# Kernel optimization log

Measured on AMD Instinct MI355X. Metric: run time of the kernel, lower is better.

Reference implementation:

```python
import jax, jax.numpy as jnp
import numpy as np

B, S, H, V = 4, 512, 256, 32000


def setup_inputs() -> dict:
    key = jax.random.key(0)
    ks = jax.random.split(key, 6)
    s = 0.02
    x = jax.random.randint(ks[0], (B, S), 0, V)
    emb = jax.random.normal(ks[1], (V, H), dtype=jnp.float32) * s
    W_ih = jax.random.normal(ks[2], (3 * H, H), dtype=jnp.float32) * s
    W_hh = jax.random.normal(ks[3], (3 * H, H), dtype=jnp.float32) * s
    b_ih = jnp.zeros((3 * H,), jnp.float32)
    b_hh = jnp.zeros((3 * H,), jnp.float32)
    W_out = jax.random.normal(ks[4], (V, H), dtype=jnp.float32) * s
    b_out = jnp.zeros((V,), jnp.float32)
    return dict(x=x, emb=emb, W_ih=W_ih, W_hh=W_hh, b_ih=b_ih, b_hh=b_hh,
                W_out=W_out, b_out=b_out)


def gru_sequence(embedded, W_ih, W_hh, b_ih, b_hh):
    # embedded: [B, S, H]; precompute all input projections once: [B, S, 3H]
    xp = jnp.einsum('bsh,gh->bsg', embedded, W_ih) + b_ih
    Hdim = W_hh.shape[1]
    h0 = jnp.zeros((embedded.shape[0], Hdim), embedded.dtype)

    def step(h, xt):  # xt: [B, 3H]
        hp = h @ W_hh.T + b_hh  # [B, 3H]
        xr, xz, xn = jnp.split(xt, 3, axis=-1)
        hr, hz, hn = jnp.split(hp, 3, axis=-1)
        r = jax.nn.sigmoid(xr + hr)
        z = jax.nn.sigmoid(xz + hz)
        n = jnp.tanh(xn + r * hn)
        h_new = (1.0 - z) * n + z * h
        return h_new, h_new

    _, hs = jax.lax.scan(step, h0, jnp.swapaxes(xp, 0, 1))  # [S, B, H]
    return jnp.swapaxes(hs, 0, 1)  # [B, S, H]


def reference(x, emb, W_ih, W_hh, b_ih, b_hh, W_out, b_out):
    embedded = emb[x]                                   # [B, S, H]
    rnn_out = gru_sequence(embedded, W_ih, W_hh, b_ih, b_hh)
    logits = jnp.einsum('bsh,vh->bsv', rnn_out, W_out) + b_out  # [B, S, V]
    # symbolic constraint: if prev token == 0, tokens >= 3 are invalid (t > 0)
    prev_zero = (x[:, :-1] == 0)                        # [B, S-1]
    prev_zero = jnp.pad(prev_zero, ((0, 0), (1, 0)))    # t=0 never masked
    vocab_ge3 = jnp.arange(logits.shape[-1]) >= 3       # [V]
    invalid = prev_zero[:, :, None] & vocab_ge3[None, None, :]
    return jnp.where(invalid, -jnp.inf, logits)
```

## Files before the change

kernel.cpp:

```cpp
#include <hip/hip_runtime.h>
#include <hip/hip_bf16.h>

typedef __attribute__((ext_vector_type(8))) short bf16x8;
typedef __attribute__((ext_vector_type(4))) float f32x4;
typedef __attribute__((ext_vector_type(2))) float f32x2;

#define HB 256
#define G3 768
#define SQ 512
#define NBATCH 4
#define NV 32000

__device__ __forceinline__ unsigned short f2bf(float f) {
    unsigned int u = __float_as_uint(f);
    u = u + 0x7FFFu + ((u >> 16) & 1u);
    return (unsigned short)(u >> 16);
}

__global__ void k_prep(const float* __restrict__ W_ih, const float* __restrict__ W_hh,
                       const float* __restrict__ W_out, float* __restrict__ w_ihT,
                       unsigned short* __restrict__ wfrag, unsigned short* __restrict__ woutbf,
                       int do_wout) {
    int stride = gridDim.x * blockDim.x;
    int tid = blockIdx.x * blockDim.x + threadIdx.x;
    for (int e = tid; e < G3 * HB; e += stride) {
        int k = e / G3, g = e - k * G3;
        w_ihT[e] = W_ih[g * HB + k];
    }
    for (int e = tid; e < G3 * HB; e += stride) {
        int i = e & 7, l = (e >> 3) & 63, c = (e >> 9) & 7, rt = (e >> 12) & 1;
        int q = e >> 13;
        int t = q % 3, w = q / 3;
        int row = t * 256 + 32 * w + 16 * rt + (l & 15);
        int kk = 32 * c + 8 * (l >> 4) + i;
        wfrag[e] = f2bf(W_hh[row * HB + kk]);
    }
    if (do_wout) {
        for (int e = tid; e < NV * HB; e += stride) woutbf[e] = f2bf(W_out[e]);
    }
}

__global__ __launch_bounds__(256) void k_embed_xp(
        const int* __restrict__ x, const float* __restrict__ emb,
        const float* __restrict__ w_ihT, const float* __restrict__ b_ih,
        const float* __restrict__ b_hh, float* __restrict__ xp) {
    __shared__ float e[8][HB];
    int tid = threadIdx.x;
    int tok0 = blockIdx.x * 8;
    {
        int s = tid >> 5, k0 = (tid & 31) * 8;
        long idx = x[tok0 + s];
        const float* src = emb + idx * (long)HB + k0;
        f32x4 a = *(const f32x4*)src, bq = *(const f32x4*)(src + 4);
        *(f32x4*)&e[s][k0] = a;
        *(f32x4*)&e[s][k0 + 4] = bq;
    }
    __syncthreads();
    #pragma unroll
    for (int it = 0; it < 3; ++it) {
        int gg = tid + it * 256;
        float acc[8] = {0.f, 0.f, 0.f, 0.f, 0.f, 0.f, 0.f, 0.f};
        for (int k = 0; k < HB; k += 4) {
            float w0 = w_ihT[(k + 0) * G3 + gg];
            float w1 = w_ihT[(k + 1) * G3 + gg];
            float w2 = w_ihT[(k + 2) * G3 + gg];
            float w3 = w_ihT[(k + 3) * G3 + gg];
            #pragma unroll
            for (int s = 0; s < 8; ++s) {
                f32x4 ev = *(const f32x4*)&e[s][k];
                acc[s] += w0 * ev.x + w1 * ev.y + w2 * ev.z + w3 * ev.w;
            }
        }
        float bias = b_ih[gg] + (gg < 512 ? b_hh[gg] : 0.f);
        #pragma unroll
        for (int s = 0; s < 8; ++s)
            xp[(size_t)(tok0 + s) * G3 + gg] = acc[s] + bias;
    }
}

__global__ __attribute__((amdgpu_waves_per_eu(2, 2))) __launch_bounds__(512)
void k_gru(const float* __restrict__ xp, const unsigned short* __restrict__ wfrag,
           const float* __restrict__ b_hh, unsigned short* __restrict__ rnn) {
    __shared__ unsigned short hbf[2][NBATCH][HB];

    int tid = threadIdx.x;
    int w = tid >> 6, l = tid & 63;
    int c15 = l & 15, hi = l >> 4;
    int b4 = c15 & 3;
    int q = c15 >> 2;
    int rt = q & 1, jh = q >> 1;
    int swz = (b4 & 1) << 6;

    bf16x8 Arz[2][2][8];
    bf16x8 An[2][8];
    #pragma unroll
    for (int g = 0; g < 2; ++g)
        #pragma unroll
        for (int r2 = 0; r2 < 2; ++r2)
            #pragma unroll
            for (int c = 0; c < 8; ++c) {
                Arz[g][r2][c] = ((const bf16x8*)wfrag)[(((w * 3 + g) * 2 + r2) * 8 + c) * 64 + l];
                asm volatile("" : "+a"(Arz[g][r2][c]));
            }
    #pragma unroll
    for (int r2 = 0; r2 < 2; ++r2)
        #pragma unroll
        for (int c = 0; c < 8; ++c) {
            An[r2][c] = ((const bf16x8*)wfrag)[(((w * 3 + 2) * 2 + r2) * 8 + c) * 64 + l];
            asm volatile("" : "+v"(An[r2][c]));
        }

    for (int k = tid; k < 2 * NBATCH * HB; k += 512) ((unsigned short*)hbf)[k] = 0;

    int row0 = 32 * w + 16 * rt + 4 * hi + 2 * jh;
    f32x2 bn = *(const f32x2*)&b_hh[512 + row0];
    float H0 = 0.f, H1 = 0.f;
    const f32x4 zz = {0.f, 0.f, 0.f, 0.f};

    const float* xpb = xp + (size_t)b4 * SQ * G3 + row0;
    unsigned short* rnb = rnn + (size_t)b4 * SQ * HB + row0;
    const char* rdb = (const char*)hbf + b4 * 512;
    char* wrb = (char*)hbf + b4 * 512 + ((row0 * 2) ^ swz);
    __syncthreads();

    for (int t = 0; t < SQ; ++t) {
        int cur = (t & 1) << 11, nxt = cur ^ 2048;

        f32x2 xr = *(const f32x2*)(xpb);
        f32x2 xz = *(const f32x2*)(xpb + 256);
        f32x2 xn = *(const f32x2*)(xpb + 512);

        f32x4 a0 = zz, a1 = zz, a2 = zz, a3 = zz, a4 = zz, a5 = zz;
        #pragma unroll
        for (int c = 0; c < 8; ++c) {
            bf16x8 Bf = *(const bf16x8*)(rdb + cur + ((64 * c + 16 * hi) ^ swz));
            asm("v_mfma_f32_16x16x32_bf16 %0, %1, %2, %0" : "+v"(a0) : "a"(Arz[0][0][c]), "v"(Bf));
            asm("v_mfma_f32_16x16x32_bf16 %0, %1, %2, %0" : "+v"(a1) : "a"(Arz[0][1][c]), "v"(Bf));
            asm("v_mfma_f32_16x16x32_bf16 %0, %1, %2, %0" : "+v"(a2) : "a"(Arz[1][0][c]), "v"(Bf));
            asm("v_mfma_f32_16x16x32_bf16 %0, %1, %2, %0" : "+v"(a3) : "a"(Arz[1][1][c]), "v"(Bf));
            a4 = __builtin_amdgcn_mfma_f32_16x16x32_bf16(An[0][c], Bf, a4, 0, 0, 0);
            a5 = __builtin_amdgcn_mfma_f32_16x16x32_bf16(An[1][c], Bf, a5, 0, 0, 0);
        }
        __builtin_amdgcn_sched_barrier(0);
        asm volatile("s_nop 7\n\ts_nop 7");
        __builtin_amdgcn_sched_barrier(0);

        bool brt = rt != 0, bjh = jh != 0;
        f32x4 vr = brt ? a1 : a0;
        f32x4 vz = brt ? a3 : a2;
        f32x4 vn = brt ? a5 : a4;
        float sr0 = bjh ? vr.z : vr.x, sr1 = bjh ? vr.w : vr.y;
        float sz0 = bjh ? vz.z : vz.x, sz1 = bjh ? vz.w : vz.y;
        float sn0 = bjh ? vn.z : vn.x, sn1 = bjh ? vn.w : vn.y;

        float r0 = __builtin_amdgcn_rcpf(1.f + __expf(-(xr.x + sr0)));
        float z0 = __builtin_amdgcn_rcpf(1.f + __expf(-(xz.x + sz0)));
        float n0 = 1.f - 2.f * __builtin_amdgcn_rcpf(__expf(2.f * (xn.x + r0 * (sn0 + bn.x))) + 1.f);
        float h0 = (1.f - z0) * n0 + z0 * H0;
        H0 = h0;
        float r1 = __builtin_amdgcn_rcpf(1.f + __expf(-(xr.y + sr1)));
        float z1 = __builtin_amdgcn_rcpf(1.f + __expf(-(xz.y + sz1)));
        float n1 = 1.f - 2.f * __builtin_amdgcn_rcpf(__expf(2.f * (xn.y + r1 * (sn1 + bn.y))) + 1.f);
        float h1 = (1.f - z1) * n1 + z1 * H1;
        H1 = h1;

        unsigned int pk;
        asm("v_cvt_pk_bf16_f32 %0, %1, %2" : "=v"(pk) : "v"(h0), "v"(h1));
        *(unsigned int*)(wrb + nxt) = pk;
        *(unsigned int*)rnb = pk;

        asm volatile("s_waitcnt lgkmcnt(0)" ::: "memory");
        __builtin_amdgcn_sched_barrier(0);
        __builtin_amdgcn_s_barrier();

        xpb += G3;
        rnb += HB;
    }
}

template <int CONV>
__global__ __launch_bounds__(256) void k_logits(
        const unsigned short* __restrict__ rnn, const unsigned short* __restrict__ woutbf,
        const float* __restrict__ woutf, const float* __restrict__ b_out,
        const int* __restrict__ x, float* __restrict__ out) {
    int tid = threadIdx.x;
    int wv = tid >> 6, l = tid & 63;
    int wm = wv >> 1, wn = wv & 1;
    int c15 = l & 15, hi = l >> 4;
    int m0 = blockIdx.y * 128 + wm * 64;
    int n0 = blockIdx.x * 128 + wn * 64;

    const f32x4 zz = {0.f, 0.f, 0.f, 0.f};
    f32x4 acc[4][4];
    #pragma unroll
    for (int i = 0; i < 4; ++i)
        #pragma unroll
        for (int j = 0; j < 4; ++j) acc[i][j] = zz;

    #pragma unroll
    for (int c = 0; c < 8; ++c) {
        bf16x8 af[4], bfr[4];
        #pragma unroll
        for (int rt = 0; rt < 4; ++rt)
            af[rt] = *(const bf16x8*)(rnn + (size_t)(m0 + rt * 16 + c15) * HB + 32 * c + 8 * hi);
        #pragma unroll
        for (int ct = 0; ct < 4; ++ct) {
            if (CONV) {
                const float* s = woutf + (size_t)(n0 + ct * 16 + c15) * HB + 32 * c + 8 * hi;
                f32x4 lo = *(const f32x4*)s, hi4 = *(const f32x4*)(s + 4);
                bf16x8 bb;
                #pragma unroll
                for (int qq = 0; qq < 4; ++qq) bb[qq] = (short)f2bf(lo[qq]);
                #pragma unroll
                for (int qq = 0; qq < 4; ++qq) bb[4 + qq] = (short)f2bf(hi4[qq]);
                bfr[ct] = bb;
            } else {
                bfr[ct] = *(const bf16x8*)(woutbf + (size_t)(n0 + ct * 16 + c15) * HB + 32 * c + 8 * hi);
            }
        }
        #pragma unroll
        for (int rt = 0; rt < 4; ++rt)
            #pragma unroll
            for (int ct = 0; ct < 4; ++ct)
                acc[rt][ct] = __builtin_amdgcn_mfma_f32_16x16x32_bf16(af[rt], bfr[ct], acc[rt][ct], 0, 0, 0);
    }

    float bo[4];
    #pragma unroll
    for (int ct = 0; ct < 4; ++ct) bo[ct] = b_out[n0 + ct * 16 + c15];

    const float NEGINF = -__builtin_inff();
    #pragma unroll
    for (int rt = 0; rt < 4; ++rt) {
        #pragma unroll
        for (int j = 0; j < 4; ++j) {
            int m = m0 + rt * 16 + 4 * hi + j;
            int tt = m & (SQ - 1);
            bool bad = (tt > 0) && (x[m - 1] == 0);
            float* orow = out + (size_t)m * NV;
            #pragma unroll
            for (int ct = 0; ct < 4; ++ct) {
                int v = n0 + ct * 16 + c15;
                float val = acc[rt][ct][j] + bo[ct];
                if (bad && v >= 3) val = NEGINF;
                orow[v] = val;
            }
        }
    }
}

extern "C" void kernel_launch(void* const* d_in, const int* in_sizes, int n_in,
                              void* d_out, int out_size, void* d_ws, size_t ws_size,
                              hipStream_t stream) {
    const int*   x     = (const int*)d_in[0];
    const float* emb   = (const float*)d_in[1];
    const float* W_ih  = (const float*)d_in[2];
    const float* W_hh  = (const float*)d_in[3];
    const float* b_ih  = (const float*)d_in[4];
    const float* b_hh  = (const float*)d_in[5];
    const float* W_out = (const float*)d_in[6];
    const float* b_out = (const float*)d_in[7];
    float* out = (float*)d_out;

    char* ws = (char*)d_ws;
    float*          xp     = (float*)(ws);
    float*          w_ihT  = (float*)(ws + 6291456);
    unsigned short* wfrag  = (unsigned short*)(ws + 7077888);
    unsigned short* rnn    = (unsigned short*)(ws + 7471104);
    unsigned short* woutbf = (unsigned short*)(ws + 8519680);
    int use_woutbf = (ws_size >= (size_t)24903680) ? 1 : 0;

    k_prep<<<2048, 256, 0, stream>>>(W_ih, W_hh, W_out, w_ihT, wfrag, woutbf, use_woutbf);
    k_embed_xp<<<256, 256, 0, stream>>>(x, emb, w_ihT, b_ih, b_hh, xp);
    k_gru<<<1, 512, 0, stream>>>(xp, wfrag, b_hh, rnn);
    dim3 g3(NV / 128, 2048 / 128);
    if (use_woutbf)
        k_logits<0><<<g3, 256, 0, stream>>>(rnn, woutbf, nullptr, b_out, x, out);
    else
        k_logits<1><<<g3, 256, 0, stream>>>(rnn, nullptr, W_out, b_out, x, out);
}
```

Baseline: 790.6 us.

## Overlap W_out bf16 conversion with GRU recurrence using extra blocks

Moves the W_out fp32-to-bf16 conversion out of the prep kernel into 64 extra blocks of the single-block GRU launch, so the conversion runs on idle CUs while the serial recurrence proceeds. It also halves tokens per block in the input-projection kernel to double its grid, shrinks the prep grid, and remaps logits blocks through a 1D grid with a swizzle across groups of eight. The risk is that the conversion blocks contend for memory bandwidth with the latency-bound GRU block, and that the swizzle changes cache reuse of W_out tiles.

```diff
diff --git a/kernel.cpp b/kernel.cpp
--- a/kernel.cpp
+++ b/kernel.cpp
@@ -4,6 +4,7 @@
 typedef __attribute__((ext_vector_type(8))) short bf16x8;
 typedef __attribute__((ext_vector_type(4))) float f32x4;
 typedef __attribute__((ext_vector_type(2))) float f32x2;
+typedef __attribute__((ext_vector_type(4))) unsigned short u16x4;
 
 #define HB 256
 #define G3 768
@@ -18,9 +19,7 @@
 }
 
 __global__ void k_prep(const float* __restrict__ W_ih, const float* __restrict__ W_hh,
-                       const float* __restrict__ W_out, float* __restrict__ w_ihT,
-                       unsigned short* __restrict__ wfrag, unsigned short* __restrict__ woutbf,
-                       int do_wout) {
+                       float* __restrict__ w_ihT, unsigned short* __restrict__ wfrag) {
     int stride = gridDim.x * blockDim.x;
     int tid = blockIdx.x * blockDim.x + threadIdx.x;
     for (int e = tid; e < G3 * HB; e += stride) {
@@ -35,19 +34,16 @@
         int kk = 32 * c + 8 * (l >> 4) + i;
         wfrag[e] = f2bf(W_hh[row * HB + kk]);
     }
-    if (do_wout) {
-        for (int e = tid; e < NV * HB; e += stride) woutbf[e] = f2bf(W_out[e]);
-    }
 }
 
 __global__ __launch_bounds__(256) void k_embed_xp(
         const int* __restrict__ x, const float* __restrict__ emb,
         const float* __restrict__ w_ihT, const float* __restrict__ b_ih,
         const float* __restrict__ b_hh, float* __restrict__ xp) {
-    __shared__ float e[8][HB];
+    __shared__ float e[4][HB];
     int tid = threadIdx.x;
-    int tok0 = blockIdx.x * 8;
-    {
+    int tok0 = blockIdx.x * 4;
+    if (tid < 128) {
         int s = tid >> 5, k0 = (tid & 31) * 8;
         long idx = x[tok0 + s];
         const float* src = emb + idx * (long)HB + k0;
@@ -59,31 +55,48 @@
     #pragma unroll
     for (int it = 0; it < 3; ++it) {
         int gg = tid + it * 256;
-        float acc[8] = {0.f, 0.f, 0.f, 0.f, 0.f, 0.f, 0.f, 0.f};
+        float acc[4] = {0.f, 0.f, 0.f, 0.f};
         for (int k = 0; k < HB; k += 4) {
             float w0 = w_ihT[(k + 0) * G3 + gg];
             float w1 = w_ihT[(k + 1) * G3 + gg];
             float w2 = w_ihT[(k + 2) * G3 + gg];
             float w3 = w_ihT[(k + 3) * G3 + gg];
             #pragma unroll
-            for (int s = 0; s < 8; ++s) {
+            for (int s = 0; s < 4; ++s) {
                 f32x4 ev = *(const f32x4*)&e[s][k];
                 acc[s] += w0 * ev.x + w1 * ev.y + w2 * ev.z + w3 * ev.w;
             }
         }
         float bias = b_ih[gg] + (gg < 512 ? b_hh[gg] : 0.f);
         #pragma unroll
-        for (int s = 0; s < 8; ++s)
+        for (int s = 0; s < 4; ++s)
             xp[(size_t)(tok0 + s) * G3 + gg] = acc[s] + bias;
     }
 }
 
 __global__ __attribute__((amdgpu_waves_per_eu(2, 2))) __launch_bounds__(512)
 void k_gru(const float* __restrict__ xp, const unsigned short* __restrict__ wfrag,
-           const float* __restrict__ b_hh, unsigned short* __restrict__ rnn) {
+           const float* __restrict__ b_hh, unsigned short* __restrict__ rnn,
+           const float* __restrict__ W_out, unsigned short* __restrict__ woutbf,
+           int do_wout) {
     __shared__ unsigned short hbf[2][NBATCH][HB];
 
     int tid = threadIdx.x;
+
+    if (blockIdx.x != 0) {
+        if (!do_wout) return;
+        int bt = (blockIdx.x - 1) * 512 + tid;
+        const f32x4* src = (const f32x4*)W_out;
+        u16x4* dst = (u16x4*)woutbf;
+        for (int qd = bt; qd < NV * HB / 4; qd += 64 * 512) {
+            f32x4 v = src[qd];
+            u16x4 o;
+            o[0] = f2bf(v.x); o[1] = f2bf(v.y); o[2] = f2bf(v.z); o[3] = f2bf(v.w);
+            dst[qd] = o;
+        }
+        return;
+    }
+
     int w = tid >> 6, l = tid & 63;
     int c15 = l & 15, hi = l >> 4;
     int b4 = c15 & 3;
@@ -183,12 +196,17 @@
         const unsigned short* __restrict__ rnn, const unsigned short* __restrict__ woutbf,
         const float* __restrict__ woutf, const float* __restrict__ b_out,
         const int* __restrict__ x, float* __restrict__ out) {
+    int fid = blockIdx.x;
+    int g = (fid & 7) * 500 + (fid >> 3);
+    int bx = g >> 4;
+    int by = g & 15;
+
     int tid = threadIdx.x;
     int wv = tid >> 6, l = tid & 63;
     int wm = wv >> 1, wn = wv & 1;
     int c15 = l & 15, hi = l >> 4;
-    int m0 = blockIdx.y * 128 + wm * 64;
-    int n0 = blockIdx.x * 128 + wn * 64;
+    int m0 = by * 128 + wm * 64;
+    int n0 = bx * 128 + wn * 64;
 
     const f32x4 zz = {0.f, 0.f, 0.f, 0.f};
     f32x4 acc[4][4];
@@ -270,12 +288,11 @@
     unsigned short* woutbf = (unsigned short*)(ws + 8519680);
     int use_woutbf = (ws_size >= (size_t)24903680) ? 1 : 0;
 
-    k_prep<<<2048, 256, 0, stream>>>(W_ih, W_hh, W_out, w_ihT, wfrag, woutbf, use_woutbf);
-    k_embed_xp<<<256, 256, 0, stream>>>(x, emb, w_ihT, b_ih, b_hh, xp);
-    k_gru<<<1, 512, 0, stream>>>(xp, wfrag, b_hh, rnn);
-    dim3 g3(NV / 128, 2048 / 128);
+    k_prep<<<512, 256, 0, stream>>>(W_ih, W_hh, w_ihT, wfrag);
+    k_embed_xp<<<512, 256, 0, stream>>>(x, emb, w_ihT, b_ih, b_hh, xp);
+    k_gru<<<65, 512, 0, stream>>>(xp, wfrag, b_hh, rnn, W_out, woutbf, use_woutbf);
     if (use_woutbf)
-        k_logits<0><<<g3, 256, 0, stream>>>(rnn, woutbf, nullptr, b_out, x, out);
+        k_logits<0><<<4000, 256, 0, stream>>>(rnn, woutbf, nullptr, b_out, x, out);
     else
-        k_logits<1><<<g3, 256, 0, stream>>>(rnn, nullptr, W_out, b_out, x, out);
-}
+        k_logits<1><<<4000, 256, 0, stream>>>(rnn, nullptr, W_out, b_out, x, out);
+}
```

Measured after the change: 753.1 us, median of 3. -4.7%, faster.
